# Performance work log

Measured on AMD Instinct MI355X. Metric: run time of the kernel, lower is better.

## Reference

```python
import jax, jax.numpy as jnp
import numpy as np

N_E = 8192
E_DIM = 255  # spatial dim; full Lorentz dim = E_DIM + 1
BETA = 0.25
EPS = 1e-7


def _rand_lorentz(key, n, d):
    """Sample n points on the Lorentz manifold (curvature c=1), radii in [1,6]."""
    k1, k2 = jax.random.split(key)
    radii = jax.random.uniform(k1, (n, 1)) * 5.0 + 1.0
    t = jnp.cosh(radii)  # time component, >= cosh(1)
    dirs = jax.random.normal(k2, (n, d))
    dirs = dirs / jnp.linalg.norm(dirs, axis=-1, keepdims=True)
    s = dirs * jnp.sqrt(jnp.maximum(t ** 2 - 1.0, 1e-7))
    return jnp.concatenate([t, s], axis=-1)


def setup_inputs() -> dict:
    key = jax.random.key(0)
    k_u, k_cb = jax.random.split(key)
    B, H, W = 8, 32, 32
    u = _rand_lorentz(k_u, B * H * W, E_DIM).reshape(B, H, W, E_DIM + 1)
    codebook = _rand_lorentz(k_cb, N_E, E_DIM)
    return {"u_hyp": u, "codebook": codebook}


def reference(u_hyp, codebook):
    shape = u_hyp.shape
    d_full = E_DIM + 1
    u = u_hyp.reshape(-1, d_full)          # [N, D]
    n = u.shape[0]
    # Minkowski metric signs: (-, +, +, ..., +)
    signs = jnp.concatenate([-jnp.ones((1,), u.dtype), jnp.ones((E_DIM,), u.dtype)])

    # Lorentzian inner products with all codes: <u, c>_L = -u0*c0 + u_s . c_s
    K = (u * signs) @ codebook.T           # [N, n_e]
    dist = jnp.arccosh(jnp.maximum(-K, 1.0 + EPS))  # hyperbolic distance (c=1)
    idx = jnp.argmin(dist, axis=-1)        # [N]
    x_q = codebook[idx]                    # [N, D] gather

    def pdist(a, b):  # elementwise Lorentzian distance
        inner = jnp.sum(a * b * signs, axis=-1)
        return jnp.arccosh(jnp.maximum(-inner, 1.0 + EPS))

    sg = jax.lax.stop_gradient
    codebook_loss = pdist(sg(u), x_q).mean()
    commitment_loss = pdist(u, sg(x_q)).mean()
    loss = codebook_loss + BETA * commitment_loss

    # straight-through estimator
    z_q = (u + sg(x_q - u)).reshape(shape)

    counts = jnp.zeros((N_E,), u.dtype).at[idx].add(1.0)
    e_mean = counts / n
    entropy = -jnp.sum(e_mean * jnp.log(e_mean + 1e-10))
    perplexity = jnp.exp(entropy)
    diversity_loss = entropy
    return loss, z_q, perplexity, diversity_loss, e_mean
```

## Files before the change

### kernel.cpp

```cpp
#include <hip/hip_runtime.h>
#include <hip/hip_bf16.h>
#include <stdint.h>

#define N_PTS   8192
#define D       256
#define N_E     8192
#define BETA    0.25f
#define EPS_1   1.0000001f

typedef unsigned long long u64;
typedef __attribute__((ext_vector_type(8))) short bf16x8;
typedef __attribute__((ext_vector_type(8))) short short8;
typedef __attribute__((ext_vector_type(4))) float f32x4;

#define WS_KEYS   0
#define WS_COUNTS (N_PTS * 8)
#define WS_LOSS   (WS_COUNTS + N_E * 4)
#define WS_AHI    (1 << 20)
#define WS_ALO    (WS_AHI + N_PTS * D * 2)
#define WS_BHI    (WS_ALO + N_PTS * D * 2)
#define WS_BLO    (WS_BHI + N_E * D * 2)

__device__ __forceinline__ short f2bf(float x) {
    __hip_bfloat16 h = __float2bfloat16(x);
    return *reinterpret_cast<short*>(&h);
}
__device__ __forceinline__ float bf2f(short s) {
    __hip_bfloat16 h = *reinterpret_cast<__hip_bfloat16*>(&s);
    return __bfloat162float(h);
}

#define GLOAD16(gp, lp) __builtin_amdgcn_global_load_lds(                      \
    (const __attribute__((address_space(1))) void*)(gp),                       \
    (__attribute__((address_space(3))) void*)(lp), 16, 0, 0)

__global__ __launch_bounds__(256) void k_prep(
    const float* __restrict__ u, const float* __restrict__ cb,
    short* __restrict__ Ahi, short* __restrict__ Alo,
    short* __restrict__ Bhi, short* __restrict__ Blo,
    u64* __restrict__ keys, float* __restrict__ counts,
    double* __restrict__ loss_sum)
{
    const int tid = blockIdx.x * 256 + threadIdx.x;
    if (tid < N_E)   counts[tid] = 0.f;
    if (tid < N_PTS) keys[tid] = ~0ULL;
    if (tid == 0)    *loss_sum = 0.0;

    const int blk = tid >> 6;
    const int l   = tid & 63;
    const int s   = blk >> 3, c = blk & 7;
    const int p   = s * 16 + (l & 15);
    const int k   = c * 32 + (l >> 4) * 8;
    const size_t gin  = (size_t)p * D + k;
    const size_t gout = (size_t)tid * 8;

    float v[8];
    short8 h8, l8;

    *(float4*)&v[0] = *(const float4*)&u[gin];
    *(float4*)&v[4] = *(const float4*)&u[gin + 4];
    if (k == 0) v[0] = -v[0];
    #pragma unroll
    for (int j = 0; j < 8; ++j) {
        h8[j] = f2bf(v[j]);
        l8[j] = f2bf(v[j] - bf2f(h8[j]));
    }
    *(short8*)&Ahi[gout] = h8;
    *(short8*)&Alo[gout] = l8;

    *(float4*)&v[0] = *(const float4*)&cb[gin];
    *(float4*)&v[4] = *(const float4*)&cb[gin + 4];
    #pragma unroll
    for (int j = 0; j < 8; ++j) {
        h8[j] = f2bf(v[j]);
        l8[j] = f2bf(v[j] - bf2f(h8[j]));
    }
    *(short8*)&Bhi[gout] = h8;
    *(short8*)&Blo[gout] = l8;
}

#define BMM 128
#define BNN 128
#define BKK 32
#define NKS (D / BKK)

__global__ __launch_bounds__(256, 4) void k_argmin_mfma(
    const short* __restrict__ Ahi, const short* __restrict__ Alo,
    const short* __restrict__ Bhi, const short* __restrict__ Blo,
    u64* __restrict__ keys)
{
    __shared__ short sm[4][8 * 512];

    const int t   = threadIdx.x;
    const int w   = t >> 6;
    const int l   = t & 63;
    const int rb  = blockIdx.x >> 6;
    const int cbk = blockIdx.x & 63;
    const int r0  = rb * BMM, c0 = cbk * BNN;
    const int wr  = w >> 1, wc = w & 1;

    const short* gsrc = (w == 0) ? Ahi : (w == 1) ? Alo : (w == 2) ? Bhi : Blo;
    short* ldst = sm[w];
    const int s0 = ((w < 2) ? rb : cbk) * 8;

    f32x4 acc[4][4];
    #pragma unroll
    for (int i = 0; i < 4; ++i)
        #pragma unroll
        for (int j = 0; j < 4; ++j) acc[i][j] = (f32x4){0.f, 0.f, 0.f, 0.f};

    for (int kk = 0; kk < NKS; ++kk) {
        __syncthreads();
        #pragma unroll
        for (int i = 0; i < 8; ++i)
            GLOAD16(gsrc + (size_t)((s0 + i) * 8 + kk) * 512 + l * 8,
                    ldst + i * 512);
        __syncthreads();

        bf16x8 ah[4], al[4], bh[4], bl[4];
        #pragma unroll
        for (int f = 0; f < 4; ++f) {
            ah[f] = *(const bf16x8*)&sm[0][(wr * 4 + f) * 512 + l * 8];
            al[f] = *(const bf16x8*)&sm[1][(wr * 4 + f) * 512 + l * 8];
            bh[f] = *(const bf16x8*)&sm[2][(wc * 4 + f) * 512 + l * 8];
            bl[f] = *(const bf16x8*)&sm[3][(wc * 4 + f) * 512 + l * 8];
        }
        #pragma unroll
        for (int mf = 0; mf < 4; ++mf)
            #pragma unroll
            for (int nf = 0; nf < 4; ++nf) {
                acc[mf][nf] = __builtin_amdgcn_mfma_f32_16x16x32_bf16(
                    ah[mf], bh[nf], acc[mf][nf], 0, 0, 0);
                acc[mf][nf] = __builtin_amdgcn_mfma_f32_16x16x32_bf16(
                    ah[mf], bl[nf], acc[mf][nf], 0, 0, 0);
                acc[mf][nf] = __builtin_amdgcn_mfma_f32_16x16x32_bf16(
                    al[mf], bh[nf], acc[mf][nf], 0, 0, 0);
            }
    }

    const int g  = l >> 4;
    const int cc = l & 15;
    #pragma unroll
    for (int mf = 0; mf < 4; ++mf) {
        #pragma unroll
        for (int r = 0; r < 4; ++r) {
            u64 km = ~0ULL;
            #pragma unroll
            for (int nf = 0; nf < 4; ++nf) {
                float m = fmaxf(-acc[mf][nf][r], EPS_1);
                unsigned code = (unsigned)(c0 + wc * 64 + nf * 16 + cc);
                u64 key = ((u64)__float_as_uint(m) << 32) | code;
                km = key < km ? key : km;
            }
            #pragma unroll
            for (int s = 8; s >= 1; s >>= 1) {
                u64 o = __shfl_xor(km, s);
                km = o < km ? o : km;
            }
            if (cc == 0)
                atomicMin(&keys[r0 + wr * 64 + mf * 16 + g * 4 + r], km);
        }
    }
}

__global__ __launch_bounds__(256) void k_gather(
    const float* __restrict__ u, const float* __restrict__ cb,
    const u64* __restrict__ keys, float* __restrict__ out,
    float* __restrict__ counts, double* __restrict__ loss_sum)
{
    __shared__ float sred[4];
    const int t    = threadIdx.x;
    const int w    = t >> 6;
    const int row  = blockIdx.x * 4 + w;
    const int lane = t & 63;
    const u64 key  = keys[row];
    const int idx  = (int)(unsigned)(key & 0xffffffffULL);

    float* zq = out + 1;
    float4 uv = *(const float4*)&u[(size_t)row * D + lane * 4];
    float4 cv = *(const float4*)&cb[(size_t)idx * D + lane * 4];
    if (lane == 0) uv.x = -uv.x;
    float partial = uv.x * cv.x + uv.y * cv.y + uv.z * cv.z + uv.w * cv.w;
    *(float4*)&zq[(size_t)row * D + lane * 4] = cv;

    #pragma unroll
    for (int s = 32; s >= 1; s >>= 1)
        partial += __shfl_xor(partial, s);

    if (lane == 0) {
        float m = fmaxf(-partial, EPS_1);
        sred[w] = acoshf(m);
        atomicAdd(&counts[idx], 1.f);
    }
    __syncthreads();
    if (t == 0)
        atomicAdd(loss_sum, (double)(sred[0] + sred[1] + sred[2] + sred[3]));
}

__global__ __launch_bounds__(256) void k_final(
    const float* __restrict__ counts, const double* __restrict__ loss_sum,
    float* __restrict__ out)
{
    __shared__ float red[256];
    const int t = threadIdx.x;
    const int OFF_P = 1 + N_PTS * D;
    float ent = 0.f;
    for (int i = t; i < N_E; i += 256) {
        float e = counts[i] * (1.0f / N_PTS);
        out[OFF_P + 2 + i] = e;
        ent -= e * logf(e + 1e-10f);
    }
    red[t] = ent;
    __syncthreads();
    for (int s = 128; s > 0; s >>= 1) {
        if (t < s) red[t] += red[t + s];
        __syncthreads();
    }
    if (t == 0) {
        float entropy = red[0];
        out[0]         = (1.0f + BETA) * (float)(*loss_sum / (double)N_PTS);
        out[OFF_P]     = expf(entropy);
        out[OFF_P + 1] = entropy;
    }
}

extern "C" void kernel_launch(void* const* d_in, const int* in_sizes, int n_in,
                              void* d_out, int out_size, void* d_ws, size_t ws_size,
                              hipStream_t stream)
{
    const float* u  = (const float*)d_in[0];
    const float* cb = (const float*)d_in[1];
    float* out = (float*)d_out;
    char* ws = (char*)d_ws;

    u64*    keys     = (u64*)(ws + WS_KEYS);
    float*  counts   = (float*)(ws + WS_COUNTS);
    double* loss_sum = (double*)(ws + WS_LOSS);
    short*  Ahi = (short*)(ws + WS_AHI);
    short*  Alo = (short*)(ws + WS_ALO);
    short*  Bhi = (short*)(ws + WS_BHI);
    short*  Blo = (short*)(ws + WS_BLO);

    k_prep<<<N_PTS * D / 8 / 256, 256, 0, stream>>>(u, cb, Ahi, Alo, Bhi, Blo,
                                                    keys, counts, loss_sum);
    k_argmin_mfma<<<(N_PTS / BMM) * (N_E / BNN), 256, 0, stream>>>(
        Ahi, Alo, Bhi, Blo, keys);
    k_gather<<<N_PTS / 4, 256, 0, stream>>>(u, cb, keys, out, counts, loss_sum);
    k_final<<<1, 256, 0, stream>>>(counts, loss_sum, out);
}
```

Before: 164.2 us.

## Enlarge argmin GEMM tiles to 256x256 and double-buffer LDS loads

The split-bf16 argmin GEMM now uses 256x256 output tiles with 512 threads (8 waves, each computing 128x64), which halves the global and LDS traffic per MFMA. LDS is double-buffered so that the next k-slice's global-to-LDS loads are issued while MFMAs run on the current slice, and one of the two __syncthreads per step is dropped. MFMA phases are wrapped in s_setprio and interleaved barriers to keep waves in lockstep. In exchange it uses 128 KB of LDS and more accumulator registers per wave, which lowers occupancy, and it launches only 1024 blocks.

```diff
diff --git a/kernel.cpp b/kernel.cpp
--- a/kernel.cpp
+++ b/kernel.cpp
@@ -79,69 +79,90 @@
     *(short8*)&Blo[gout] = l8;
 }
 
-#define BMM 128
-#define BNN 128
-#define BKK 32
-#define NKS (D / BKK)
-
-__global__ __launch_bounds__(256, 4) void k_argmin_mfma(
+#define BMM 256
+#define BNN 256
+#define NKS 8
+
+__global__ __launch_bounds__(512, 2) void k_argmin_mfma(
     const short* __restrict__ Ahi, const short* __restrict__ Alo,
     const short* __restrict__ Bhi, const short* __restrict__ Blo,
     u64* __restrict__ keys)
 {
-    __shared__ short sm[4][8 * 512];
-
-    const int t   = threadIdx.x;
-    const int w   = t >> 6;
-    const int l   = t & 63;
-    const int rb  = blockIdx.x >> 6;
-    const int cbk = blockIdx.x & 63;
-    const int r0  = rb * BMM, c0 = cbk * BNN;
-    const int wr  = w >> 1, wc = w & 1;
-
-    const short* gsrc = (w == 0) ? Ahi : (w == 1) ? Alo : (w == 2) ? Bhi : Blo;
-    short* ldst = sm[w];
-    const int s0 = ((w < 2) ? rb : cbk) * 8;
-
-    f32x4 acc[4][4];
-    #pragma unroll
-    for (int i = 0; i < 4; ++i)
+    __shared__ short sm[2][4][16 * 512];
+
+    const int t    = threadIdx.x;
+    const int w    = t >> 6;
+    const int l    = t & 63;
+    const int rb   = blockIdx.x >> 5;
+    const int cbk  = blockIdx.x & 31;
+    const int r0   = rb * BMM, c0 = cbk * BNN;
+    const int wr   = w >> 2, wc = w & 3;
+
+    const int a    = w & 3;
+    const int half = w >> 2;
+    const short* gsrc = (a == 0) ? Ahi : (a == 1) ? Alo : (a == 2) ? Bhi : Blo;
+    const int ab   = ((a < 2) ? rb : cbk) * 16 + half * 8;
+
+    f32x4 acc[8][4];
+    #pragma unroll
+    for (int i = 0; i < 8; ++i)
         #pragma unroll
         for (int j = 0; j < 4; ++j) acc[i][j] = (f32x4){0.f, 0.f, 0.f, 0.f};
 
+    #pragma unroll
+    for (int i = 0; i < 8; ++i)
+        GLOAD16(gsrc + ((size_t)(ab + i) * 8 + 0) * 512 + l * 8,
+                &sm[0][a][(half * 8 + i) * 512]);
+
     for (int kk = 0; kk < NKS; ++kk) {
+        const int c = kk & 1;
         __syncthreads();
-        #pragma unroll
-        for (int i = 0; i < 8; ++i)
-            GLOAD16(gsrc + (size_t)((s0 + i) * 8 + kk) * 512 + l * 8,
-                    ldst + i * 512);
-        __syncthreads();
-
-        bf16x8 ah[4], al[4], bh[4], bl[4];
-        #pragma unroll
-        for (int f = 0; f < 4; ++f) {
-            ah[f] = *(const bf16x8*)&sm[0][(wr * 4 + f) * 512 + l * 8];
-            al[f] = *(const bf16x8*)&sm[1][(wr * 4 + f) * 512 + l * 8];
-            bh[f] = *(const bf16x8*)&sm[2][(wc * 4 + f) * 512 + l * 8];
-            bl[f] = *(const bf16x8*)&sm[3][(wc * 4 + f) * 512 + l * 8];
-        }
-        #pragma unroll
-        for (int mf = 0; mf < 4; ++mf)
-            #pragma unroll
-            for (int nf = 0; nf < 4; ++nf) {
-                acc[mf][nf] = __builtin_amdgcn_mfma_f32_16x16x32_bf16(
-                    ah[mf], bh[nf], acc[mf][nf], 0, 0, 0);
-                acc[mf][nf] = __builtin_amdgcn_mfma_f32_16x16x32_bf16(
-                    ah[mf], bl[nf], acc[mf][nf], 0, 0, 0);
-                acc[mf][nf] = __builtin_amdgcn_mfma_f32_16x16x32_bf16(
-                    al[mf], bh[nf], acc[mf][nf], 0, 0, 0);
-            }
+
+        if (kk < NKS - 1) {
+            #pragma unroll
+            for (int i = 0; i < 8; ++i)
+                GLOAD16(gsrc + ((size_t)(ab + i) * 8 + kk + 1) * 512 + l * 8,
+                        &sm[c ^ 1][a][(half * 8 + i) * 512]);
+        }
+
+        bf16x8 bh[4], bl[4];
+        #pragma unroll
+        for (int nf = 0; nf < 4; ++nf) {
+            bh[nf] = *(const bf16x8*)&sm[c][2][(wc * 4 + nf) * 512 + l * 8];
+            bl[nf] = *(const bf16x8*)&sm[c][3][(wc * 4 + nf) * 512 + l * 8];
+        }
+        #pragma unroll
+        for (int ph = 0; ph < 4; ++ph) {
+            bf16x8 ah[2], al[2];
+            #pragma unroll
+            for (int q = 0; q < 2; ++q) {
+                const int mf = ph * 2 + q;
+                ah[q] = *(const bf16x8*)&sm[c][0][(wr * 8 + mf) * 512 + l * 8];
+                al[q] = *(const bf16x8*)&sm[c][1][(wr * 8 + mf) * 512 + l * 8];
+            }
+            __builtin_amdgcn_s_setprio(1);
+            #pragma unroll
+            for (int q = 0; q < 2; ++q) {
+                const int mf = ph * 2 + q;
+                #pragma unroll
+                for (int nf = 0; nf < 4; ++nf) {
+                    acc[mf][nf] = __builtin_amdgcn_mfma_f32_16x16x32_bf16(
+                        ah[q], bh[nf], acc[mf][nf], 0, 0, 0);
+                    acc[mf][nf] = __builtin_amdgcn_mfma_f32_16x16x32_bf16(
+                        ah[q], bl[nf], acc[mf][nf], 0, 0, 0);
+                    acc[mf][nf] = __builtin_amdgcn_mfma_f32_16x16x32_bf16(
+                        al[q], bh[nf], acc[mf][nf], 0, 0, 0);
+                }
+            }
+            __builtin_amdgcn_s_setprio(0);
+            if (ph < 3) __builtin_amdgcn_s_barrier();
+        }
     }
 
     const int g  = l >> 4;
     const int cc = l & 15;
     #pragma unroll
-    for (int mf = 0; mf < 4; ++mf) {
+    for (int mf = 0; mf < 8; ++mf) {
         #pragma unroll
         for (int r = 0; r < 4; ++r) {
             u64 km = ~0ULL;
@@ -158,7 +179,7 @@
                 km = o < km ? o : km;
             }
             if (cc == 0)
-                atomicMin(&keys[r0 + wr * 64 + mf * 16 + g * 4 + r], km);
+                atomicMin(&keys[r0 + wr * 128 + mf * 16 + g * 4 + r], km);
         }
     }
 }
@@ -243,7 +264,7 @@
 
     k_prep<<<N_PTS * D / 8 / 256, 256, 0, stream>>>(u, cb, Ahi, Alo, Bhi, Blo,
                                                     keys, counts, loss_sum);
-    k_argmin_mfma<<<(N_PTS / BMM) * (N_E / BNN), 256, 0, stream>>>(
+    k_argmin_mfma<<<(N_PTS / BMM) * (N_E / BNN), 512, 0, stream>>>(
         Ahi, Alo, Bhi, Blo, keys);
     k_gather<<<N_PTS / 4, 256, 0, stream>>>(u, cb, keys, out, counts, loss_sum);
     k_final<<<1, 256, 0, stream>>>(counts, loss_sum, out);
```

After: 184.6 us. 12.4% more time.

## Switch argmin GEMM to 32x32 MFMA tiles with double-buffered LDS prefetch

Applied to the files above, without the earlier changes.

The prep kernel now packs the bf16 hi/lo operands in 32x16 fragment order, and the argmin kernel uses 32x32x16 MFMA instructions on 2x2 fragment tiles per wave instead of 4x4 tiles of 16x16x32. The K loop uses a double-buffered LDS layout so the next K slice is loaded while the current one feeds the MFMAs, which removes one barrier per step. The MFMA section also raises wave priority. The LDS footprint doubles and launch bounds drop to two blocks per CU, so occupancy falls and the epilogue reduction needs more shuffle steps.

```diff
diff --git a/kernel.cpp b/kernel.cpp
--- a/kernel.cpp
+++ b/kernel.cpp
@@ -9,9 +9,9 @@
 #define EPS_1   1.0000001f
 
 typedef unsigned long long u64;
-typedef __attribute__((ext_vector_type(8))) short bf16x8;
-typedef __attribute__((ext_vector_type(8))) short short8;
-typedef __attribute__((ext_vector_type(4))) float f32x4;
+typedef __attribute__((ext_vector_type(8)))  short bf16x8;
+typedef __attribute__((ext_vector_type(8)))  short short8;
+typedef __attribute__((ext_vector_type(16))) float f32x16;
 
 #define WS_KEYS   0
 #define WS_COUNTS (N_PTS * 8)
@@ -46,11 +46,10 @@
     if (tid < N_PTS) keys[tid] = ~0ULL;
     if (tid == 0)    *loss_sum = 0.0;
 
-    const int blk = tid >> 6;
-    const int l   = tid & 63;
-    const int s   = blk >> 3, c = blk & 7;
-    const int p   = s * 16 + (l & 15);
-    const int k   = c * 32 + (l >> 4) * 8;
+    const int fi = tid >> 6;
+    const int l  = tid & 63;
+    const int p  = (fi >> 4) * 32 + (l & 31);
+    const int k  = (fi & 15) * 16 + (l >> 5) * 8;
     const size_t gin  = (size_t)p * D + k;
     const size_t gout = (size_t)tid * 8;
 
@@ -81,15 +80,14 @@
 
 #define BMM 128
 #define BNN 128
-#define BKK 32
-#define NKS (D / BKK)
-
-__global__ __launch_bounds__(256, 4) void k_argmin_mfma(
+#define NKS 8
+
+__global__ __launch_bounds__(256, 2) void k_argmin_mfma(
     const short* __restrict__ Ahi, const short* __restrict__ Alo,
     const short* __restrict__ Bhi, const short* __restrict__ Blo,
     u64* __restrict__ keys)
 {
-    __shared__ short sm[4][8 * 512];
+    __shared__ short sm[2][4][8 * 512];
 
     const int t   = threadIdx.x;
     const int w   = t >> 6;
@@ -100,65 +98,83 @@
     const int wr  = w >> 1, wc = w & 1;
 
     const short* gsrc = (w == 0) ? Ahi : (w == 1) ? Alo : (w == 2) ? Bhi : Blo;
-    short* ldst = sm[w];
-    const int s0 = ((w < 2) ? rb : cbk) * 8;
-
-    f32x4 acc[4][4];
-    #pragma unroll
-    for (int i = 0; i < 4; ++i)
-        #pragma unroll
-        for (int j = 0; j < 4; ++j) acc[i][j] = (f32x4){0.f, 0.f, 0.f, 0.f};
+    const int eb = ((w < 2) ? rb : cbk) * 4;
+
+    f32x16 acc[2][2];
+    #pragma unroll
+    for (int i = 0; i < 2; ++i)
+        #pragma unroll
+        for (int j = 0; j < 2; ++j)
+            #pragma unroll
+            for (int r = 0; r < 16; ++r) acc[i][j][r] = 0.f;
+
+    #pragma unroll
+    for (int i = 0; i < 8; ++i)
+        GLOAD16(gsrc + ((size_t)(eb + (i >> 1)) * 16 + (i & 1)) * 512 + l * 8,
+                &sm[0][w][i * 512]);
+    __syncthreads();
 
     for (int kk = 0; kk < NKS; ++kk) {
+        const int c = kk & 1;
+        if (kk + 1 < NKS) {
+            #pragma unroll
+            for (int i = 0; i < 8; ++i)
+                GLOAD16(gsrc + ((size_t)(eb + (i >> 1)) * 16 +
+                                (kk + 1) * 2 + (i & 1)) * 512 + l * 8,
+                        &sm[c ^ 1][w][i * 512]);
+        }
+
+        bf16x8 ah[2][2], al[2][2], bh[2][2], bl[2][2];
+        #pragma unroll
+        for (int m = 0; m < 2; ++m)
+            #pragma unroll
+            for (int kf = 0; kf < 2; ++kf) {
+                ah[m][kf] = *(const bf16x8*)&sm[c][0][((wr*2+m)*2+kf)*512 + l*8];
+                al[m][kf] = *(const bf16x8*)&sm[c][1][((wr*2+m)*2+kf)*512 + l*8];
+                bh[m][kf] = *(const bf16x8*)&sm[c][2][((wc*2+m)*2+kf)*512 + l*8];
+                bl[m][kf] = *(const bf16x8*)&sm[c][3][((wc*2+m)*2+kf)*512 + l*8];
+            }
+        __builtin_amdgcn_s_setprio(1);
+        #pragma unroll
+        for (int kf = 0; kf < 2; ++kf)
+            #pragma unroll
+            for (int m = 0; m < 2; ++m)
+                #pragma unroll
+                for (int n = 0; n < 2; ++n) {
+                    acc[m][n] = __builtin_amdgcn_mfma_f32_32x32x16_bf16(
+                        ah[m][kf], bh[n][kf], acc[m][n], 0, 0, 0);
+                    acc[m][n] = __builtin_amdgcn_mfma_f32_32x32x16_bf16(
+                        ah[m][kf], bl[n][kf], acc[m][n], 0, 0, 0);
+                    acc[m][n] = __builtin_amdgcn_mfma_f32_32x32x16_bf16(
+                        al[m][kf], bh[n][kf], acc[m][n], 0, 0, 0);
+                }
+        __builtin_amdgcn_s_setprio(0);
         __syncthreads();
-        #pragma unroll
-        for (int i = 0; i < 8; ++i)
-            GLOAD16(gsrc + (size_t)((s0 + i) * 8 + kk) * 512 + l * 8,
-                    ldst + i * 512);
-        __syncthreads();
-
-        bf16x8 ah[4], al[4], bh[4], bl[4];
-        #pragma unroll
-        for (int f = 0; f < 4; ++f) {
-            ah[f] = *(const bf16x8*)&sm[0][(wr * 4 + f) * 512 + l * 8];
-            al[f] = *(const bf16x8*)&sm[1][(wr * 4 + f) * 512 + l * 8];
-            bh[f] = *(const bf16x8*)&sm[2][(wc * 4 + f) * 512 + l * 8];
-            bl[f] = *(const bf16x8*)&sm[3][(wc * 4 + f) * 512 + l * 8];
-        }
-        #pragma unroll
-        for (int mf = 0; mf < 4; ++mf)
-            #pragma unroll
-            for (int nf = 0; nf < 4; ++nf) {
-                acc[mf][nf] = __builtin_amdgcn_mfma_f32_16x16x32_bf16(
-                    ah[mf], bh[nf], acc[mf][nf], 0, 0, 0);
-                acc[mf][nf] = __builtin_amdgcn_mfma_f32_16x16x32_bf16(
-                    ah[mf], bl[nf], acc[mf][nf], 0, 0, 0);
-                acc[mf][nf] = __builtin_amdgcn_mfma_f32_16x16x32_bf16(
-                    al[mf], bh[nf], acc[mf][nf], 0, 0, 0);
-            }
-    }
-
-    const int g  = l >> 4;
-    const int cc = l & 15;
-    #pragma unroll
-    for (int mf = 0; mf < 4; ++mf) {
-        #pragma unroll
-        for (int r = 0; r < 4; ++r) {
+    }
+
+    const int ch = l & 31;
+    #pragma unroll
+    for (int m = 0; m < 2; ++m) {
+        #pragma unroll
+        for (int r = 0; r < 16; ++r) {
             u64 km = ~0ULL;
             #pragma unroll
-            for (int nf = 0; nf < 4; ++nf) {
-                float m = fmaxf(-acc[mf][nf][r], EPS_1);
-                unsigned code = (unsigned)(c0 + wc * 64 + nf * 16 + cc);
-                u64 key = ((u64)__float_as_uint(m) << 32) | code;
+            for (int n = 0; n < 2; ++n) {
+                float mm = fmaxf(-acc[m][n][r], EPS_1);
+                unsigned code = (unsigned)(c0 + wc * 64 + n * 32 + ch);
+                u64 key = ((u64)__float_as_uint(mm) << 32) | code;
                 km = key < km ? key : km;
             }
             #pragma unroll
-            for (int s = 8; s >= 1; s >>= 1) {
+            for (int s = 16; s >= 1; s >>= 1) {
                 u64 o = __shfl_xor(km, s);
                 km = o < km ? o : km;
             }
-            if (cc == 0)
-                atomicMin(&keys[r0 + wr * 64 + mf * 16 + g * 4 + r], km);
+            if (ch == 0) {
+                const int row = r0 + wr * 64 + m * 32 +
+                                (r & 3) + 8 * (r >> 2) + 4 * (l >> 5);
+                atomicMin(&keys[row], km);
+            }
         }
     }
 }
```

After: 234.7 us. +42.9%, slower.
